# Kernel optimization log

Hardware: AMD Instinct MI355X
Metric: run time of the kernel (lower is better)

## Reference

```python
import jax, jax.numpy as jnp
import numpy as np

N = 100000      # nodes
E = 1600000     # edges (avg degree 16)
DIN = 32        # input feature dim
H = 16          # nhidden
DEPTH = 4       # number of SAGEConv layers


def setup_inputs() -> dict:
    key = jax.random.key(0)
    ks = jax.random.split(key, 16)
    s = 0.1
    inp = {
        "x": jax.random.normal(ks[0], (N, DIN), jnp.float32),
        "edge_index": jax.random.randint(ks[1], (2, E), 0, N, dtype=jnp.int64),
        # SAGEConv layer 0: in=DIN -> out=H. lin_l has bias, lin_r has no bias (PyG default).
        "Wl0": jax.random.normal(ks[2], (H, DIN), jnp.float32) * s,
        "bl0": jnp.zeros((H,), jnp.float32),
        "Wr0": jax.random.normal(ks[3], (H, DIN), jnp.float32) * s,
        # SAGEConv layers 1..3: in=H -> out=H, stacked.
        "Wls": jax.random.normal(ks[4], (DEPTH - 1, H, H), jnp.float32) * s,
        "bls": jnp.zeros((DEPTH - 1, H), jnp.float32),
        "Wrs": jax.random.normal(ks[5], (DEPTH - 1, H, H), jnp.float32) * s,
        # lin_out MLP: [H, 2H, 2H, 1] with acts [silu, silu, None], no batch norm.
        "W1": jax.random.normal(ks[6], (2 * H, H), jnp.float32) * s,
        "b1": jnp.zeros((2 * H,), jnp.float32),
        "W2": jax.random.normal(ks[7], (2 * H, 2 * H), jnp.float32) * s,
        "b2": jnp.zeros((2 * H,), jnp.float32),
        "W3": jax.random.normal(ks[8], (1, 2 * H), jnp.float32) * s,
        "b3": jnp.zeros((1,), jnp.float32),
    }
    return inp


def reference(x, edge_index, Wl0, bl0, Wr0, Wls, bls, Wrs, W1, b1, W2, b2, W3, b3):
    src = edge_index[0]  # message source (x_j)
    dst = edge_index[1]  # aggregation target (x_i)

    def sage(h, Wl, bl, Wr):
        # sum-aggregate neighbor features, then lin_l(agg) + lin_r(h)
        agg = jax.ops.segment_sum(h[src], dst, num_segments=N)  # [N, d]
        return agg @ Wl.T + bl + h @ Wr.T

    x = jax.nn.silu(sage(x, Wl0, bl0, Wr0))
    for i in range(DEPTH - 1):
        x = jax.nn.silu(sage(x, Wls[i], bls[i], Wrs[i]))

    out = jax.nn.silu(x @ W1.T + b1)
    out = jax.nn.silu(out @ W2.T + b2)
    out = out @ W3.T + b3  # [N, 1]
    return out
```

## Files before the change

kernel.cpp:

```cpp
#include <hip/hip_runtime.h>


#define SH      8
#define BWID    256
#define NBK     512
#define CHUNK   4096
#define EPT     (CHUNK / 256)
#define SUBCAP  48
#define BCAP    5120

__device__ __forceinline__ float silu_f(float v) {
    return v * __builtin_amdgcn_rcpf(1.0f + __expf(-v));
}

__device__ __forceinline__ float bf_lo(unsigned u) { return __uint_as_float(u << 16); }
__device__ __forceinline__ float bf_hi(unsigned u) { return __uint_as_float(u & 0xFFFF0000u); }
__device__ __forceinline__ unsigned short f2bf(float f) {
    unsigned x = __float_as_uint(f);
    unsigned r = x + 0x7FFFu + ((x >> 16) & 1u);
    return (unsigned short)(r >> 16);
}
__device__ __forceinline__ unsigned pack_bf2(float a, float b) {
    return (unsigned)f2bf(a) | ((unsigned)f2bf(b) << 16);
}


__global__ __launch_bounds__(256) void bin_dense0(
    const int* __restrict__ src, const int* __restrict__ dst,
    unsigned short* __restrict__ cnt16,
    unsigned* __restrict__ binned0,
    const float* __restrict__ x,
    const float* __restrict__ Wl0, const float* __restrict__ bl0,
    const float* __restrict__ Wr0,
    unsigned* __restrict__ hlb, float* __restrict__ acc,
    int n, int ne, int nblocks)
{
    __shared__ int   s_hist[NBK];
    __shared__ float sWl[512], sWr[512], sbl[16];

    const int t = threadIdx.x;
    const int blk = blockIdx.x;
    for (int i = t; i < 512; i += 256) { sWl[i] = Wl0[i]; sWr[i] = Wr0[i]; }
    if (t < 16) sbl[t] = bl0[t];

    const int base = blk * CHUNK;
    const int cnt = min(CHUNK, ne - base);

    int es[EPT], ed[EPT];
#pragma unroll
    for (int j = 0; j < EPT; ++j) {
        const int i = t + j * 256;
        if (i < cnt) { es[j] = src[base + i]; ed[j] = dst[base + i]; }
        else         { es[j] = -1; ed[j] = -1; }
    }

    s_hist[t] = 0; s_hist[t + 256] = 0;
    __syncthreads();
#pragma unroll
    for (int j = 0; j < EPT; ++j)
        if (es[j] >= 0) atomicAdd(&s_hist[ed[j] >> SH], 1);
    __syncthreads();

    cnt16[blk * NBK + t]       = (unsigned short)s_hist[t];
    cnt16[blk * NBK + t + 256] = (unsigned short)s_hist[t + 256];
    s_hist[t] = 0; s_hist[t + 256] = 0;
    __syncthreads();

#pragma unroll
    for (int j = 0; j < EPT; ++j) {
        if (es[j] >= 0) {
            const int b  = ed[j] >> SH;
            const int ld = ed[j] & (BWID - 1);
            const int r  = atomicAdd(&s_hist[b], 1);
            if (r < SUBCAP)
                binned0[((size_t)b * nblocks + blk) * SUBCAP + r] =
                    ((unsigned)ld << 17) | (unsigned)es[j];
        }
    }

    const int node = blk * 256 + t;
    if (node >= n) return;

    float h[32];
    const float4* __restrict__ xp = (const float4*)(x + (size_t)node * 32);
#pragma unroll
    for (int r = 0; r < 8; ++r) {
        const float4 vv = xp[r];
        h[4*r+0] = vv.x; h[4*r+1] = vv.y; h[4*r+2] = vv.z; h[4*r+3] = vv.w;
    }

    const float4* __restrict__ sWl4 = (const float4*)sWl;
    const float4* __restrict__ sWr4 = (const float4*)sWr;
    float ol[16], oa[16];
#pragma unroll
    for (int j = 0; j < 16; ++j) {
        float al = 0.f, ar = 0.f;
#pragma unroll
        for (int d4 = 0; d4 < 8; ++d4) {
            const float4 wl = sWl4[j * 8 + d4];
            const float4 wr = sWr4[j * 8 + d4];
            al = fmaf(wl.x, h[4*d4+0], al); al = fmaf(wl.y, h[4*d4+1], al);
            al = fmaf(wl.z, h[4*d4+2], al); al = fmaf(wl.w, h[4*d4+3], al);
            ar = fmaf(wr.x, h[4*d4+0], ar); ar = fmaf(wr.y, h[4*d4+1], ar);
            ar = fmaf(wr.z, h[4*d4+2], ar); ar = fmaf(wr.w, h[4*d4+3], ar);
        }
        ol[j] = al;
        oa[j] = sbl[j] + ar;
    }

    unsigned u[8];
#pragma unroll
    for (int r = 0; r < 8; ++r) u[r] = pack_bf2(ol[2*r], ol[2*r+1]);
    uint4* __restrict__ hp = (uint4*)(hlb + (size_t)node * 8);
    hp[0] = make_uint4(u[0], u[1], u[2], u[3]);
    hp[1] = make_uint4(u[4], u[5], u[6], u[7]);
    float4* __restrict__ ap = (float4*)(acc + (size_t)node * 16);
#pragma unroll
    for (int r = 0; r < 4; ++r)
        ap[r] = make_float4(oa[4*r], oa[4*r+1], oa[4*r+2], oa[4*r+3]);
}

__global__ __launch_bounds__(512) void node_sort(
    const unsigned* __restrict__ binned0,
    const unsigned short* __restrict__ cnt16,
    int* __restrict__ binned1,
    int2* __restrict__ noff2,
    int n, int nblocks)
{
    __shared__ int cnt[BWID];
    __shared__ int off_[BWID];
    __shared__ unsigned short s_cnt[512];
    const int b = blockIdx.x, t = threadIdx.x;
    const int dbase = b * BCAP;
    const unsigned* __restrict__ seg = binned0 + (size_t)b * nblocks * SUBCAP;

    for (int i = t; i < nblocks; i += 512) s_cnt[i] = cnt16[i * NBK + b];
    if (t < BWID) cnt[t] = 0;
    __syncthreads();

    const int tot = nblocks * SUBCAP;
    for (int idx = t; idx < tot; idx += 512) {
        const int i = idx / SUBCAP, r = idx % SUBCAP;
        if (r < (int)s_cnt[i]) atomicAdd(&cnt[seg[idx] >> 17], 1);
    }
    __syncthreads();

    if (t < BWID) off_[t] = cnt[t];
    __syncthreads();
    for (int o = 1; o < BWID; o <<= 1) {
        const int add = (t < BWID && t >= o) ? off_[t - o] : 0;
        __syncthreads();
        if (t < BWID) off_[t] += add;
        __syncthreads();
    }
    if (t < BWID) off_[t] -= cnt[t];
    __syncthreads();

    if (t < BWID) {
        const int node = (b << SH) + t;
        if (node < n)
            noff2[node] = make_int2(dbase + off_[t], dbase + off_[t] + cnt[t]);
        cnt[t] = 0;
    }
    __syncthreads();

    for (int idx = t; idx < tot; idx += 512) {
        const int i = idx / SUBCAP, r = idx % SUBCAP;
        if (r < (int)s_cnt[i]) {
            const unsigned u = seg[idx];
            const int ld = (int)(u >> 17);
            const int r2 = atomicAdd(&cnt[ld], 1);
            binned1[dbase + off_[ld] + r2] = (int)(u & 0x1FFFFu);
        }
    }
}


__device__ __forceinline__ void gather16_4(
    const int* __restrict__ binned1, const uint4* __restrict__ h4,
    int beg, int end, int q, float* p)
{
#pragma unroll
    for (int i = 0; i < 16; ++i) p[i] = 0.f;
    int k = beg + q;
    for (; k + 4 < end; k += 8) {
        const int s0 = binned1[k];
        const int s1 = binned1[k + 4];
        const uint4 a0 = h4[(size_t)s0 * 2];
        const uint4 a1 = h4[(size_t)s0 * 2 + 1];
        const uint4 b0 = h4[(size_t)s1 * 2];
        const uint4 b1 = h4[(size_t)s1 * 2 + 1];
        p[0] += bf_lo(a0.x); p[1] += bf_hi(a0.x); p[2] += bf_lo(a0.y); p[3] += bf_hi(a0.y);
        p[4] += bf_lo(a0.z); p[5] += bf_hi(a0.z); p[6] += bf_lo(a0.w); p[7] += bf_hi(a0.w);
        p[8] += bf_lo(a1.x); p[9] += bf_hi(a1.x); p[10]+= bf_lo(a1.y); p[11]+= bf_hi(a1.y);
        p[12]+= bf_lo(a1.z); p[13]+= bf_hi(a1.z); p[14]+= bf_lo(a1.w); p[15]+= bf_hi(a1.w);
        p[0] += bf_lo(b0.x); p[1] += bf_hi(b0.x); p[2] += bf_lo(b0.y); p[3] += bf_hi(b0.y);
        p[4] += bf_lo(b0.z); p[5] += bf_hi(b0.z); p[6] += bf_lo(b0.w); p[7] += bf_hi(b0.w);
        p[8] += bf_lo(b1.x); p[9] += bf_hi(b1.x); p[10]+= bf_lo(b1.y); p[11]+= bf_hi(b1.y);
        p[12]+= bf_lo(b1.z); p[13]+= bf_hi(b1.z); p[14]+= bf_lo(b1.w); p[15]+= bf_hi(b1.w);
    }
    if (k < end) {
        const int s0 = binned1[k];
        const uint4 a0 = h4[(size_t)s0 * 2];
        const uint4 a1 = h4[(size_t)s0 * 2 + 1];
        p[0] += bf_lo(a0.x); p[1] += bf_hi(a0.x); p[2] += bf_lo(a0.y); p[3] += bf_hi(a0.y);
        p[4] += bf_lo(a0.z); p[5] += bf_hi(a0.z); p[6] += bf_lo(a0.w); p[7] += bf_hi(a0.w);
        p[8] += bf_lo(a1.x); p[9] += bf_hi(a1.x); p[10]+= bf_lo(a1.y); p[11]+= bf_hi(a1.y);
        p[12]+= bf_lo(a1.z); p[13]+= bf_hi(a1.z); p[14]+= bf_lo(a1.w); p[15]+= bf_hi(a1.w);
    }
#pragma unroll
    for (int i = 0; i < 16; ++i) p[i] += __shfl_xor(p[i], 1);
#pragma unroll
    for (int i = 0; i < 16; ++i) p[i] += __shfl_xor(p[i], 2);
}

__global__ __launch_bounds__(256, 4) void fused_agg_dense(
    const int2* __restrict__ noff2, const int* __restrict__ binned1,
    const unsigned* __restrict__ hl_in, const float* __restrict__ acc_in,
    const float* __restrict__ Wl, const float* __restrict__ bl,
    const float* __restrict__ Wr,
    unsigned* __restrict__ hl_out, float* __restrict__ acc_out, int n)
{
    __shared__ float sWl[256], sWr[256], sbl[16];
    const int t = threadIdx.x;
    sWl[t] = Wl[t]; sWr[t] = Wr[t];
    if (t < 16) sbl[t] = bl[t];
    __syncthreads();

    const int gid = blockIdx.x * 256 + t;
    const int node = gid >> 2;
    if (node >= n) return;
    const int q = t & 3;
    const int2 be = noff2[node];

    float p[16];
    gather16_4(binned1, (const uint4*)hl_in, be.x, be.y, q, p);

    const float4* __restrict__ ai = (const float4*)(acc_in + (size_t)node * 16);
    float h[16];
#pragma unroll
    for (int r = 0; r < 4; ++r) {
        const float4 a = ai[r];
        h[4*r+0] = silu_f(a.x + p[4*r+0]);
        h[4*r+1] = silu_f(a.y + p[4*r+1]);
        h[4*r+2] = silu_f(a.z + p[4*r+2]);
        h[4*r+3] = silu_f(a.w + p[4*r+3]);
    }

    const float4* __restrict__ sWl4 = (const float4*)sWl;
    const float4* __restrict__ sWr4 = (const float4*)sWr;
    float ol[4], oa[4];
#pragma unroll
    for (int jj = 0; jj < 4; ++jj) {
        const int j = 4 * q + jj;
        float al = 0.f, ar = 0.f;
#pragma unroll
        for (int d4 = 0; d4 < 4; ++d4) {
            const float4 wl = sWl4[j * 4 + d4];
            const float4 wr = sWr4[j * 4 + d4];
            al = fmaf(wl.x, h[4*d4+0], al); al = fmaf(wl.y, h[4*d4+1], al);
            al = fmaf(wl.z, h[4*d4+2], al); al = fmaf(wl.w, h[4*d4+3], al);
            ar = fmaf(wr.x, h[4*d4+0], ar); ar = fmaf(wr.y, h[4*d4+1], ar);
            ar = fmaf(wr.z, h[4*d4+2], ar); ar = fmaf(wr.w, h[4*d4+3], ar);
        }
        ol[jj] = al;
        oa[jj] = sbl[j] + ar;
    }

    ((uint2*)hl_out)[(size_t)node * 4 + q] =
        make_uint2(pack_bf2(ol[0], ol[1]), pack_bf2(ol[2], ol[3]));
    ((float4*)acc_out)[(size_t)node * 4 + q] =
        make_float4(oa[0], oa[1], oa[2], oa[3]);
}

__global__ __launch_bounds__(256, 3) void fused_agg_mlp(
    const int2* __restrict__ noff2, const int* __restrict__ binned1,
    const unsigned* __restrict__ hl_in, const float* __restrict__ acc_in,
    const float* __restrict__ W1, const float* __restrict__ b1,
    const float* __restrict__ W2, const float* __restrict__ b2,
    const float* __restrict__ W3, const float* __restrict__ b3,
    float* __restrict__ out, int n)
{
    __shared__ float sW1[512], sW2[1024], sb1[32], sb2[32], sW3[32];
    __shared__ float sb3;
    const int t = threadIdx.x;
    for (int i = t; i < 512; i += 256) sW1[i] = W1[i];
    for (int i = t; i < 1024; i += 256) sW2[i] = W2[i];
    if (t < 32) { sb1[t] = b1[t]; sb2[t] = b2[t]; sW3[t] = W3[t]; }
    if (t == 0) sb3 = b3[0];
    __syncthreads();

    const int gid = blockIdx.x * 256 + t;
    const int node = gid >> 2;
    if (node >= n) return;
    const int q = t & 3;
    const int2 be = noff2[node];

    float p[16];
    gather16_4(binned1, (const uint4*)hl_in, be.x, be.y, q, p);

    const float4* __restrict__ ai = (const float4*)(acc_in + (size_t)node * 16);
    float h[16];
#pragma unroll
    for (int r = 0; r < 4; ++r) {
        const float4 a = ai[r];
        h[4*r+0] = silu_f(a.x + p[4*r+0]);
        h[4*r+1] = silu_f(a.y + p[4*r+1]);
        h[4*r+2] = silu_f(a.z + p[4*r+2]);
        h[4*r+3] = silu_f(a.w + p[4*r+3]);
    }

    const float4* __restrict__ sW1v = (const float4*)sW1;
    float a1[8];
#pragma unroll
    for (int jj = 0; jj < 8; ++jj) {
        const int j = 8 * q + jj;
        float s = sb1[j];
#pragma unroll
        for (int d4 = 0; d4 < 4; ++d4) {
            const float4 w = sW1v[j * 4 + d4];
            s = fmaf(w.x, h[4*d4+0], s); s = fmaf(w.y, h[4*d4+1], s);
            s = fmaf(w.z, h[4*d4+2], s); s = fmaf(w.w, h[4*d4+3], s);
        }
        a1[jj] = silu_f(s);
    }

    float t0[16];
#pragma unroll
    for (int i = 0; i < 8; ++i) {
        const float mine  = a1[i];
        const float other = __shfl_xor(mine, 1);
        const bool hi = (q & 1);
        t0[i]     = hi ? other : mine;
        t0[8 + i] = hi ? mine  : other;
    }
    float A1[32];
#pragma unroll
    for (int i = 0; i < 16; ++i) {
        const float mine  = t0[i];
        const float other = __shfl_xor(mine, 2);
        const bool hi = (q & 2);
        A1[i]      = hi ? other : mine;
        A1[16 + i] = hi ? mine  : other;
    }

    const float4* __restrict__ sW2v = (const float4*)sW2;
    float part = 0.f;
#pragma unroll
    for (int jj = 0; jj < 8; ++jj) {
        const int j = 8 * q + jj;
        float s = sb2[j];
#pragma unroll
        for (int d4 = 0; d4 < 8; ++d4) {
            const float4 w = sW2v[j * 8 + d4];
            s = fmaf(w.x, A1[4*d4+0], s); s = fmaf(w.y, A1[4*d4+1], s);
            s = fmaf(w.z, A1[4*d4+2], s); s = fmaf(w.w, A1[4*d4+3], s);
        }
        part = fmaf(sW3[j], silu_f(s), part);
    }
    part += __shfl_xor(part, 1);
    part += __shfl_xor(part, 2);
    if (q == 0) out[node] = part + sb3;
}

extern "C" void kernel_launch(void* const* d_in, const int* in_sizes, int n_in,
                              void* d_out, int out_size, void* d_ws, size_t ws_size,
                              hipStream_t stream)
{
    const float* x   = (const float*)d_in[0];
    const int*   ei  = (const int*)d_in[1];
    const float* Wl0 = (const float*)d_in[2];
    const float* bl0 = (const float*)d_in[3];
    const float* Wr0 = (const float*)d_in[4];
    const float* Wls = (const float*)d_in[5];
    const float* bls = (const float*)d_in[6];
    const float* Wrs = (const float*)d_in[7];
    const float* W1  = (const float*)d_in[8];
    const float* b1  = (const float*)d_in[9];
    const float* W2  = (const float*)d_in[10];
    const float* b2  = (const float*)d_in[11];
    const float* W3  = (const float*)d_in[12];
    const float* b3  = (const float*)d_in[13];

    const int n  = in_sizes[0] / 32;
    const int ne = in_sizes[1] / 2;
    const int* src = ei;
    const int* dst = ei + ne;
    const int nbuck   = (n + BWID - 1) >> SH;
    const int nblocks = (ne + CHUNK - 1) / CHUNK;

    float*    acc0    = (float*)d_ws;
    float*    acc1    = acc0 + (size_t)n * 16;
    unsigned* hlbA    = (unsigned*)(acc1 + (size_t)n * 16);
    unsigned* hlbB    = hlbA + (size_t)n * 8;
    int2*     noff2   = (int2*)(hlbB + (size_t)n * 8);
    int*      binned1 = (int*)(noff2 + n);
    unsigned short* cnt16 = (unsigned short*)(binned1 + (size_t)nbuck * BCAP);
    unsigned* binned0 = (unsigned*)(cnt16 + (size_t)nblocks * NBK);

    const int lb = (n * 4 + 255) / 256;

    bin_dense0<<<nblocks, 256, 0, stream>>>(src, dst, cnt16, binned0,
                                            x, Wl0, bl0, Wr0, hlbA, acc0,
                                            n, ne, nblocks);
    node_sort<<<nbuck, 512, 0, stream>>>(binned0, cnt16, binned1, noff2,
                                         n, nblocks);

    fused_agg_dense<<<lb, 256, 0, stream>>>(noff2, binned1, hlbA, acc0,
        Wls + 0,   bls + 0,  Wrs + 0,   hlbB, acc1, n);
    fused_agg_dense<<<lb, 256, 0, stream>>>(noff2, binned1, hlbB, acc1,
        Wls + 256, bls + 16, Wrs + 256, hlbA, acc0, n);
    fused_agg_dense<<<lb, 256, 0, stream>>>(noff2, binned1, hlbA, acc0,
        Wls + 512, bls + 32, Wrs + 512, hlbB, acc1, n);
    fused_agg_mlp<<<lb, 256, 0, stream>>>(noff2, binned1, hlbB, acc1,
        W1, b1, W2, b2, W3, b3, (float*)d_out, n);
}
```

Measured before the change: 162.9 us.

## Locally sort edges per chunk in shared memory and write compact bucket runs

The binning kernel now prefix-sums its per-bucket histogram and scatters each chunk's edges into a shared-memory buffer ordered by bucket. It then writes that buffer to global memory contiguously and records per-bucket offsets in a new scan16 array. This replaces the padded SUBCAP slot layout with its scattered global writes and silent overflow truncation. node_sort now walks variable-length per-chunk runs using those offsets instead of scanning all padded slots. CHUNK is halved so the extra shared buffer fits, and the dense part uses 128 nodes per block; in exchange, node_sort's per-thread serial run loops are less coalesced and less balanced.

Result: no change. 164.0 us (+0.7%).

```diff
diff --git a/kernel.cpp b/kernel.cpp
--- a/kernel.cpp
+++ b/kernel.cpp
@@ -4,9 +4,8 @@
 #define SH      8
 #define BWID    256
 #define NBK     512
-#define CHUNK   4096
+#define CHUNK   2048
 #define EPT     (CHUNK / 256)
-#define SUBCAP  48
 #define BCAP    5120
 
 __device__ __forceinline__ float silu_f(float v) {
@@ -28,6 +27,7 @@
 __global__ __launch_bounds__(256) void bin_dense0(
     const int* __restrict__ src, const int* __restrict__ dst,
     unsigned short* __restrict__ cnt16,
+    unsigned short* __restrict__ scan16,
     unsigned* __restrict__ binned0,
     const float* __restrict__ x,
     const float* __restrict__ Wl0, const float* __restrict__ bl0,
@@ -35,8 +35,11 @@
     unsigned* __restrict__ hlb, float* __restrict__ acc,
     int n, int ne, int nblocks)
 {
-    __shared__ int   s_hist[NBK];
-    __shared__ float sWl[512], sWr[512], sbl[16];
+    __shared__ int      s_hist[NBK];
+    __shared__ int      s_off[NBK];
+    __shared__ int      s_p[256];
+    __shared__ unsigned s_items[CHUNK];
+    __shared__ float    sWl[512], sWr[512], sbl[16];
 
     const int t = threadIdx.x;
     const int blk = blockIdx.x;
@@ -61,10 +64,28 @@
         if (es[j] >= 0) atomicAdd(&s_hist[ed[j] >> SH], 1);
     __syncthreads();
 
-    cnt16[blk * NBK + t]       = (unsigned short)s_hist[t];
-    cnt16[blk * NBK + t + 256] = (unsigned short)s_hist[t + 256];
+    const int c0 = s_hist[2 * t], c1 = s_hist[2 * t + 1];
+    const int ps = c0 + c1;
+    s_p[t] = ps;
+    __syncthreads();
+    int v = ps;
+    for (int o = 1; o < 256; o <<= 1) {
+        const int add = (t >= o) ? s_p[t - o] : 0;
+        __syncthreads();
+        v += add;
+        s_p[t] = v;
+        __syncthreads();
+    }
+    const int ex = v - ps;
+    s_off[2 * t] = ex;
+    s_off[2 * t + 1] = ex + c0;
+
+    cnt16[blk * NBK + t]        = (unsigned short)s_hist[t];
+    cnt16[blk * NBK + t + 256]  = (unsigned short)s_hist[t + 256];
     s_hist[t] = 0; s_hist[t + 256] = 0;
     __syncthreads();
+    scan16[blk * NBK + t]       = (unsigned short)s_off[t];
+    scan16[blk * NBK + t + 256] = (unsigned short)s_off[t + 256];
 
 #pragma unroll
     for (int j = 0; j < EPT; ++j) {
@@ -72,13 +93,16 @@
             const int b  = ed[j] >> SH;
             const int ld = ed[j] & (BWID - 1);
             const int r  = atomicAdd(&s_hist[b], 1);
-            if (r < SUBCAP)
-                binned0[((size_t)b * nblocks + blk) * SUBCAP + r] =
-                    ((unsigned)ld << 17) | (unsigned)es[j];
-        }
-    }
-
-    const int node = blk * 256 + t;
+            s_items[s_off[b] + r] = ((unsigned)ld << 17) | (unsigned)es[j];
+        }
+    }
+    __syncthreads();
+
+    for (int i = t; i < cnt; i += 256)
+        binned0[base + i] = s_items[i];
+
+    if (t >= 128) return;
+    const int node = blk * 128 + t;
     if (node >= n) return;
 
     float h[32];
@@ -123,25 +147,25 @@
 __global__ __launch_bounds__(512) void node_sort(
     const unsigned* __restrict__ binned0,
     const unsigned short* __restrict__ cnt16,
+    const unsigned short* __restrict__ scan16,
     int* __restrict__ binned1,
     int2* __restrict__ noff2,
     int n, int nblocks)
 {
     __shared__ int cnt[BWID];
     __shared__ int off_[BWID];
-    __shared__ unsigned short s_cnt[512];
     const int b = blockIdx.x, t = threadIdx.x;
     const int dbase = b * BCAP;
-    const unsigned* __restrict__ seg = binned0 + (size_t)b * nblocks * SUBCAP;
-
-    for (int i = t; i < nblocks; i += 512) s_cnt[i] = cnt16[i * NBK + b];
+
     if (t < BWID) cnt[t] = 0;
     __syncthreads();
 
-    const int tot = nblocks * SUBCAP;
-    for (int idx = t; idx < tot; idx += 512) {
-        const int i = idx / SUBCAP, r = idx % SUBCAP;
-        if (r < (int)s_cnt[i]) atomicAdd(&cnt[seg[idx] >> 17], 1);
+    for (int i = t; i < nblocks; i += 512) {
+        const int c = cnt16[i * NBK + b];
+        const int s = scan16[i * NBK + b];
+        const unsigned* __restrict__ run = binned0 + (size_t)i * CHUNK + s;
+        for (int r = 0; r < c; ++r)
+            atomicAdd(&cnt[run[r] >> 17], 1);
     }
     __syncthreads();
 
@@ -164,10 +188,12 @@
     }
     __syncthreads();
 
-    for (int idx = t; idx < tot; idx += 512) {
-        const int i = idx / SUBCAP, r = idx % SUBCAP;
-        if (r < (int)s_cnt[i]) {
-            const unsigned u = seg[idx];
+    for (int i = t; i < nblocks; i += 512) {
+        const int c = cnt16[i * NBK + b];
+        const int s = scan16[i * NBK + b];
+        const unsigned* __restrict__ run = binned0 + (size_t)i * CHUNK + s;
+        for (int r = 0; r < c; ++r) {
+            const unsigned u = run[r];
             const int ld = (int)(u >> 17);
             const int r2 = atomicAdd(&cnt[ld], 1);
             binned1[dbase + off_[ld] + r2] = (int)(u & 0x1FFFFu);
@@ -395,15 +421,16 @@
     unsigned* hlbB    = hlbA + (size_t)n * 8;
     int2*     noff2   = (int2*)(hlbB + (size_t)n * 8);
     int*      binned1 = (int*)(noff2 + n);
-    unsigned short* cnt16 = (unsigned short*)(binned1 + (size_t)nbuck * BCAP);
-    unsigned* binned0 = (unsigned*)(cnt16 + (size_t)nblocks * NBK);
+    unsigned short* cnt16  = (unsigned short*)(binned1 + (size_t)nbuck * BCAP);
+    unsigned short* scan16 = cnt16 + (size_t)nblocks * NBK;
+    unsigned* binned0 = (unsigned*)(scan16 + (size_t)nblocks * NBK);
 
     const int lb = (n * 4 + 255) / 256;
 
-    bin_dense0<<<nblocks, 256, 0, stream>>>(src, dst, cnt16, binned0,
+    bin_dense0<<<nblocks, 256, 0, stream>>>(src, dst, cnt16, scan16, binned0,
                                             x, Wl0, bl0, Wr0, hlbA, acc0,
                                             n, ne, nblocks);
-    node_sort<<<nbuck, 512, 0, stream>>>(binned0, cnt16, binned1, noff2,
+    node_sort<<<nbuck, 512, 0, stream>>>(binned0, cnt16, scan16, binned1, noff2,
                                          n, nblocks);
 
     fused_agg_dense<<<lb, 256, 0, stream>>>(noff2, binned1, hlbA, acc0,
```
